# Kernel tuning notes

Measured on AMD Instinct MI355X. Metric: run time of the kernel, lower is better.

The kernel has to match this reference:

```python
import jax, jax.numpy as jnp
import numpy as np
import math

B, T, C = 2, 2048, 768
NH, HD = 12, 64  # n_head, head_dim

def setup_inputs() -> dict:
    key = jax.random.key(0)
    k1, k2, k3 = jax.random.split(key, 3)
    x = jax.random.normal(k1, (B, T, C), dtype=jnp.float32)
    mask = jnp.tril(jnp.ones((T, T), dtype=bool))[None, None]  # [1,1,T,T] causal
    Wqkv = jax.random.normal(k2, (C, 3 * C), dtype=jnp.float32) * (1.0 / math.sqrt(C))
    Wproj = jax.random.normal(k3, (C, C), dtype=jnp.float32) * (1.0 / math.sqrt(C))
    return {"x": x, "mask": mask, "Wqkv": Wqkv, "Wproj": Wproj}

def reference(x, mask, Wqkv, Wproj):
    b, t, c = x.shape
    qkv = x @ Wqkv  # [b,t,3c]
    q, k, v = jnp.split(qkv, 3, axis=-1)
    q = q.reshape(b, t, NH, HD).transpose(0, 2, 1, 3)  # [b,h,t,d]
    k = k.reshape(b, t, NH, HD).transpose(0, 2, 1, 3)
    v = v.reshape(b, t, NH, HD).transpose(0, 2, 1, 3)
    att = jnp.einsum('bhqd,bhkd->bhqk', q, k) / math.sqrt(HD)
    att = jnp.where(mask, att, -jnp.inf)
    att = jax.nn.softmax(att, axis=-1)
    out = jnp.einsum('bhqk,bhkd->bhqd', att, v)
    out = out.transpose(0, 2, 1, 3).reshape(b, t, c)
    return out @ Wproj
```

## Files before the change

### kernel.cpp

```cpp
#include <hip/hip_runtime.h>
#include <hip/hip_bf16.h>

#define T_   2048
#define C_   768
#define NH_  12
#define HD_  64
#define M_   (2*T_)
#define N1_  (3*C_)
#define PB_  ((size_t)NH_*T_*HD_)
#define KS_  0.180336880f

typedef __attribute__((ext_vector_type(8))) short  short8;
typedef __attribute__((ext_vector_type(4))) float  floatx4;

__device__ __forceinline__ floatx4 mfma_bf16(short8 a, short8 b, floatx4 c) {
    return __builtin_amdgcn_mfma_f32_16x16x32_bf16(a, b, c, 0, 0, 0);
}
__device__ __forceinline__ float fast_exp2(float x) {
    return __builtin_amdgcn_exp2f(x);
}

__global__ __launch_bounds__(256) void gemm_xw(const void* __restrict__ A,
                                               const float* __restrict__ Bf,
                                               int a_is_f32, int row0, int N, int K,
                                               int mode, int orow0,
                                               void* __restrict__ O0,
                                               __hip_bfloat16* __restrict__ O1,
                                               __hip_bfloat16* __restrict__ O2) {
    __shared__ __align__(16) __hip_bfloat16 As[128 * 40];
    __shared__ __align__(16) __hip_bfloat16 Bs[128 * 40];

    const int tid  = threadIdx.x;
    const int n0   = blockIdx.x * 128;
    const int m0   = blockIdx.y * 128;
    const int srow = tid >> 1;
    const int scol = (tid & 1) * 16;
    const int bn   = tid & 127;
    const int bg   = tid >> 7;
    const int wave = tid >> 6;
    const int ln   = tid & 63;
    const int l16  = ln & 15;
    const int q4   = ln >> 4;
    const int wm   = (wave >> 1) * 64;
    const int wn   = (wave & 1) * 64;

    floatx4 acc[4][4];
#pragma unroll
    for (int i = 0; i < 4; i++)
#pragma unroll
        for (int j = 0; j < 4; j++) acc[i][j] = (floatx4){0.f, 0.f, 0.f, 0.f};

    const size_t arow = (size_t)(row0 + m0 + srow) * K;

    for (int k0 = 0; k0 < K; k0 += 32) {
        union { __hip_bfloat16 h[16]; short8 v[2]; } au, bu;
        if (a_is_f32) {
            const float* Af = (const float*)A;
            const size_t base = arow + k0 + scol;
            floatx4 f0 = *(const floatx4*)(Af + base);
            floatx4 f1 = *(const floatx4*)(Af + base + 4);
            floatx4 f2 = *(const floatx4*)(Af + base + 8);
            floatx4 f3 = *(const floatx4*)(Af + base + 12);
#pragma unroll
            for (int j = 0; j < 4; j++) {
                au.h[j]      = __float2bfloat16(f0[j]);
                au.h[4 + j]  = __float2bfloat16(f1[j]);
                au.h[8 + j]  = __float2bfloat16(f2[j]);
                au.h[12 + j] = __float2bfloat16(f3[j]);
            }
        } else {
            const __hip_bfloat16* Ab = (const __hip_bfloat16*)A;
            au.v[0] = *(const short8*)(Ab + arow + k0 + scol);
            au.v[1] = *(const short8*)(Ab + arow + k0 + scol + 8);
        }
#pragma unroll
        for (int j = 0; j < 16; j++)
            bu.h[j] = __float2bfloat16(Bf[(size_t)(k0 + bg * 16 + j) * N + n0 + bn]);
        __syncthreads();
        *(short8*)(As + srow * 40 + scol)     = au.v[0];
        *(short8*)(As + srow * 40 + scol + 8) = au.v[1];
        *(short8*)(Bs + bn * 40 + bg * 16)     = bu.v[0];
        *(short8*)(Bs + bn * 40 + bg * 16 + 8) = bu.v[1];
        __syncthreads();
        short8 af[4], bfr[4];
#pragma unroll
        for (int i = 0; i < 4; i++) {
            af[i]  = *(const short8*)(As + (wm + i * 16 + l16) * 40 + q4 * 8);
            bfr[i] = *(const short8*)(Bs + (wn + i * 16 + l16) * 40 + q4 * 8);
        }
#pragma unroll
        for (int i = 0; i < 4; i++)
#pragma unroll
            for (int j = 0; j < 4; j++)
                acc[i][j] = mfma_bf16(af[i], bfr[j], acc[i][j]);
    }

#pragma unroll
    for (int i = 0; i < 4; i++) {
        const int mbase = m0 + wm + i * 16 + q4 * 4;
#pragma unroll
        for (int j = 0; j < 4; j++) {
            const int n = n0 + wn + j * 16 + l16;
#pragma unroll
            for (int r = 0; r < 4; r++) {
                const int mm = mbase + r;
                const float fv = acc[i][j][r];
                if (mode == 1) {
                    ((float*)O0)[(size_t)(orow0 + mm) * N + n] = fv;
                } else {
                    const __hip_bfloat16 hv = __float2bfloat16(fv);
                    const int which = n / C_;
                    const int rem   = n - which * C_;
                    const int h     = rem >> 6;
                    const int d     = rem & 63;
                    const int bh    = (mm >> 11) * NH_ + h;
                    const int t     = mm & (T_ - 1);
                    if (which == 0)      ((__hip_bfloat16*)O0)[((size_t)bh * T_ + t) * HD_ + d] = hv;
                    else if (which == 1) O1[((size_t)bh * T_ + t) * HD_ + d] = hv;
                    else                 O2[((size_t)bh * HD_ + d) * T_ + t] = hv;
                }
            }
        }
    }
}

__global__ __launch_bounds__(128) void attn_fused(const __hip_bfloat16* __restrict__ Q,
                                                  const __hip_bfloat16* __restrict__ Kd,
                                                  const __hip_bfloat16* __restrict__ Vt,
                                                  __hip_bfloat16* __restrict__ O) {
    __shared__ __align__(16) __hip_bfloat16 plds[2][2][16][72];
    __shared__ __align__(16) floatx4 accbuf[2][4][64];
    __shared__ float mbuf[2][16], lbuf[2][16];

    const int bh   = blockIdx.x;
    const int wid  = threadIdx.x >> 6;
    const int lane = threadIdx.x & 63;
    const int l16  = lane & 15;
    const int q4   = lane >> 4;
    const int i    = 63 - (int)blockIdx.y;
    const int q0A  = 32 * i;
    const int q0B  = 32 * i + 16;
    const int nch  = (i >> 1) + 1;

    const __hip_bfloat16* Qh = Q  + (size_t)bh * T_ * HD_;
    const __hip_bfloat16* Kh = Kd + (size_t)bh * T_ * HD_;
    const __hip_bfloat16* Vh = Vt + (size_t)bh * HD_ * T_;

    short8 aqA[2], aqB[2];
#pragma unroll
    for (int kt = 0; kt < 2; kt++) {
        aqA[kt] = *(const short8*)(Qh + (size_t)(q0A + l16) * HD_ + kt * 32 + q4 * 8);
        aqB[kt] = *(const short8*)(Qh + (size_t)(q0B + l16) * HD_ + kt * 32 + q4 * 8);
    }

    floatx4 accA[4], accB[4];
#pragma unroll
    for (int ct = 0; ct < 4; ct++) {
        accA[ct] = (floatx4){0.f, 0.f, 0.f, 0.f};
        accB[ct] = (floatx4){0.f, 0.f, 0.f, 0.f};
    }
    float mA[4], lA[4], mB[4], lB[4];
#pragma unroll
    for (int r = 0; r < 4; r++) { mA[r] = mB[r] = -3e38f; lA[r] = lB[r] = 0.f; }

    for (int c = wid; c < nch; c += 2) {
        const int kv0 = c * 64;
        const bool diag = (c == nch - 1);

        short8 bk[4][2];
#pragma unroll
        for (int nt = 0; nt < 4; nt++)
#pragma unroll
            for (int kt = 0; kt < 2; kt++)
                bk[nt][kt] = *(const short8*)(Kh + (size_t)(kv0 + nt * 16 + l16) * HD_ + kt * 32 + q4 * 8);

        floatx4 sA[4], sB[4];
#pragma unroll
        for (int nt = 0; nt < 4; nt++) {
            sA[nt] = (floatx4){0.f, 0.f, 0.f, 0.f};
            sB[nt] = (floatx4){0.f, 0.f, 0.f, 0.f};
#pragma unroll
            for (int kt = 0; kt < 2; kt++) {
                sA[nt] = mfma_bf16(aqA[kt], bk[nt][kt], sA[nt]);
                sB[nt] = mfma_bf16(aqB[kt], bk[nt][kt], sB[nt]);
            }
        }

        if (diag) {
#pragma unroll
            for (int r = 0; r < 4; r++) {
#pragma unroll
                for (int nt = 0; nt < 4; nt++) {
                    const int kvc = kv0 + nt * 16 + l16;
                    if (kvc > q0A + q4 * 4 + r) sA[nt][r] = -3e38f;
                    if (kvc > q0B + q4 * 4 + r) sB[nt][r] = -3e38f;
                }
            }
        }

        float mxA[4], mxB[4];
#pragma unroll
        for (int r = 0; r < 4; r++) {
            mxA[r] = fmaxf(fmaxf(sA[0][r], sA[1][r]), fmaxf(sA[2][r], sA[3][r]));
            mxB[r] = fmaxf(fmaxf(sB[0][r], sB[1][r]), fmaxf(sB[2][r], sB[3][r]));
        }
#pragma unroll
        for (int off = 1; off < 16; off <<= 1)
#pragma unroll
            for (int r = 0; r < 4; r++) {
                mxA[r] = fmaxf(mxA[r], __shfl_xor(mxA[r], off, 64));
                mxB[r] = fmaxf(mxB[r], __shfl_xor(mxB[r], off, 64));
            }

        float rsA[4], rsB[4], alA[4], alB[4];
#pragma unroll
        for (int r = 0; r < 4; r++) {
            const float mnA = fmaxf(mA[r], mxA[r]);
            const float mnB = fmaxf(mB[r], mxB[r]);
            alA[r] = fast_exp2((mA[r] - mnA) * KS_);
            alB[r] = fast_exp2((mB[r] - mnB) * KS_);
            mA[r] = mnA; mB[r] = mnB;
            const float mkA = mnA * KS_, mkB = mnB * KS_;
            float ra = 0.f, rb = 0.f;
#pragma unroll
            for (int nt = 0; nt < 4; nt++) {
                const float pa = fast_exp2(sA[nt][r] * KS_ - mkA);
                const float pb = fast_exp2(sB[nt][r] * KS_ - mkB);
                plds[wid][0][q4 * 4 + r][nt * 16 + l16] = __float2bfloat16(pa);
                plds[wid][1][q4 * 4 + r][nt * 16 + l16] = __float2bfloat16(pb);
                ra += pa; rb += pb;
            }
            rsA[r] = ra; rsB[r] = rb;
        }
#pragma unroll
        for (int off = 1; off < 16; off <<= 1)
#pragma unroll
            for (int r = 0; r < 4; r++) {
                rsA[r] += __shfl_xor(rsA[r], off, 64);
                rsB[r] += __shfl_xor(rsB[r], off, 64);
            }
#pragma unroll
        for (int r = 0; r < 4; r++) {
            lA[r] = alA[r] * lA[r] + rsA[r];
            lB[r] = alB[r] * lB[r] + rsB[r];
        }
#pragma unroll
        for (int ct = 0; ct < 4; ct++)
#pragma unroll
            for (int r = 0; r < 4; r++) {
                accA[ct][r] *= alA[r];
                accB[ct][r] *= alB[r];
            }

        __threadfence_block();

        short8 apA[2], apB[2];
#pragma unroll
        for (int kt = 0; kt < 2; kt++) {
            apA[kt] = *(const short8*)(&plds[wid][0][l16][kt * 32 + q4 * 8]);
            apB[kt] = *(const short8*)(&plds[wid][1][l16][kt * 32 + q4 * 8]);
        }
#pragma unroll
        for (int ct = 0; ct < 4; ct++)
#pragma unroll
            for (int kt = 0; kt < 2; kt++) {
                short8 bv = *(const short8*)(Vh + (size_t)(ct * 16 + l16) * T_ + kv0 + kt * 32 + q4 * 8);
                accA[ct] = mfma_bf16(apA[kt], bv, accA[ct]);
                accB[ct] = mfma_bf16(apB[kt], bv, accB[ct]);
            }

        __threadfence_block();
    }

    __syncthreads();
    if (wid == 0) {
        if (l16 == 0)
#pragma unroll
            for (int r = 0; r < 4; r++) { mbuf[1][q4 * 4 + r] = mB[r]; lbuf[1][q4 * 4 + r] = lB[r]; }
#pragma unroll
        for (int ct = 0; ct < 4; ct++) accbuf[1][ct][lane] = accB[ct];
    } else {
        if (l16 == 0)
#pragma unroll
            for (int r = 0; r < 4; r++) { mbuf[0][q4 * 4 + r] = mA[r]; lbuf[0][q4 * 4 + r] = lA[r]; }
#pragma unroll
        for (int ct = 0; ct < 4; ct++) accbuf[0][ct][lane] = accA[ct];
    }
    __syncthreads();

    const int orow0 = (bh / NH_) * T_;
    const int hcol  = (bh % NH_) * HD_;
    const int slot  = wid;
    const int q0    = wid ? q0B : q0A;
#pragma unroll
    for (int r = 0; r < 4; r++) {
        const float m0v = wid ? mB[r] : mA[r];
        const float l0v = wid ? lB[r] : lA[r];
        const float m1v = mbuf[slot][q4 * 4 + r];
        const float l1v = lbuf[slot][q4 * 4 + r];
        const float ms  = fmaxf(m0v, m1v);
        const float w0  = fast_exp2((m0v - ms) * KS_);
        const float w1  = fast_exp2((m1v - ms) * KS_);
        const float inv = 1.0f / (l0v * w0 + l1v * w1);
        __hip_bfloat16* orow = O + (size_t)(orow0 + q0 + q4 * 4 + r) * C_ + hcol;
#pragma unroll
        for (int ct = 0; ct < 4; ct++) {
            const float a0 = wid ? accB[ct][r] : accA[ct][r];
            const float a1 = accbuf[slot][ct][lane][r];
            orow[ct * 16 + l16] = __float2bfloat16((a0 * w0 + a1 * w1) * inv);
        }
    }
}

extern "C" void kernel_launch(void* const* d_in, const int* in_sizes, int n_in,
                              void* d_out, int out_size, void* d_ws, size_t ws_size,
                              hipStream_t stream) {
    const float *x = nullptr, *wqkv = nullptr, *wproj = nullptr;
    for (int i = 0; i < n_in; i++) {
        const int s = in_sizes[i];
        if (s == M_ * C_ && !x) x = (const float*)d_in[i];
        else if (s == C_ * N1_ && !wqkv) wqkv = (const float*)d_in[i];
        else if (s == C_ * C_ && !wproj) wproj = (const float*)d_in[i];
    }
    float* out = (float*)d_out;
    __hip_bfloat16* ws = (__hip_bfloat16*)d_ws;
    __hip_bfloat16* Vt = (__hip_bfloat16*)d_out;

    const size_t needB = 6 * PB_ * 2;
    if (ws_size >= needB) {
        __hip_bfloat16* Qall = ws;
        __hip_bfloat16* Kall = Qall + 2 * PB_;
        __hip_bfloat16* ATT  = Kall + 2 * PB_;
        gemm_xw<<<dim3(N1_ / 128, M_ / 128), 256, 0, stream>>>(
            x, wqkv, 1, 0, N1_, C_, 0, 0, (void*)Qall, Kall, Vt);
        attn_fused<<<dim3(2 * NH_, 64), 128, 0, stream>>>(Qall, Kall, Vt, ATT);
        gemm_xw<<<dim3(C_ / 128, M_ / 128), 256, 0, stream>>>(
            ATT, wproj, 0, 0, C_, C_, 1, 0, (void*)out, nullptr, nullptr);
    } else {
        __hip_bfloat16* Qb      = ws;
        __hip_bfloat16* Kb      = Qb + PB_;
        __hip_bfloat16* ATTb[2] = {Kb + PB_, Kb + 2 * PB_};
        for (int b = 0; b < 2; b++) {
            __hip_bfloat16* Vtb = Vt + (size_t)b * PB_;
            gemm_xw<<<dim3(N1_ / 128, T_ / 128), 256, 0, stream>>>(
                x, wqkv, 1, b * T_, N1_, C_, 0, 0, (void*)Qb, Kb, Vtb);
            attn_fused<<<dim3(NH_, 64), 128, 0, stream>>>(Qb, Kb, Vtb, ATTb[b]);
        }
        for (int b = 0; b < 2; b++)
            gemm_xw<<<dim3(C_ / 128, T_ / 128), 256, 0, stream>>>(
                ATTb[b], wproj, 0, 0, C_, C_, 1, b * T_, (void*)out, nullptr, nullptr);
    }
}
```

Before: 212.9 us.

## Pre-convert inputs to bf16, add transposed-B GEMMs, split attention across four waves

Adds prep kernels that convert x to bf16 and transpose-convert both weight matrices to bf16, so the GEMMs load contiguous bf16 rows and skip the per-tile strided fp32 weight reads and conversions. The QKV GEMM becomes a 128x128 transposed-B kernel and the output projection a 64x64 tile kernel for more blocks. Attention goes from two to four waves per block with a tree merge of partial softmax states through reused LDS. The cost is extra launches and extra global traffic for the converted copies, which are stored in reused workspace and output buffers.

```diff
diff --git a/kernel.cpp b/kernel.cpp
--- a/kernel.cpp
+++ b/kernel.cpp
@@ -11,6 +11,7 @@
 #define KS_  0.180336880f
 
 typedef __attribute__((ext_vector_type(8))) short  short8;
+typedef __attribute__((ext_vector_type(4))) short  shortx4;
 typedef __attribute__((ext_vector_type(4))) float  floatx4;
 
 __device__ __forceinline__ floatx4 mfma_bf16(short8 a, short8 b, floatx4 c) {
@@ -18,6 +19,185 @@
 }
 __device__ __forceinline__ float fast_exp2(float x) {
     return __builtin_amdgcn_exp2f(x);
+}
+
+__global__ __launch_bounds__(256) void prep1(const float* __restrict__ x,
+                                             const float* __restrict__ wqkv,
+                                             __hip_bfloat16* __restrict__ xb,
+                                             __hip_bfloat16* __restrict__ wqkvT) {
+    if (blockIdx.x < 3072) {
+        const int idx = blockIdx.x * 256 + threadIdx.x;
+        const floatx4 v = ((const floatx4*)x)[idx];
+        union { __hip_bfloat16 h[4]; shortx4 s; } u;
+#pragma unroll
+        for (int j = 0; j < 4; j++) u.h[j] = __float2bfloat16(v[j]);
+        ((shortx4*)xb)[idx] = u.s;
+    } else {
+        const int j  = (blockIdx.x - 3072) * 256 + threadIdx.x;
+        const int k8 = j / N1_;
+        const int n  = j - k8 * N1_;
+        union { __hip_bfloat16 h[8]; short8 s; } u;
+#pragma unroll
+        for (int jj = 0; jj < 8; jj++)
+            u.h[jj] = __float2bfloat16(wqkv[(size_t)(k8 * 8 + jj) * N1_ + n]);
+        *(short8*)(wqkvT + (size_t)n * C_ + k8 * 8) = u.s;
+    }
+}
+
+__global__ __launch_bounds__(256) void prep2(const float* __restrict__ wproj,
+                                             __hip_bfloat16* __restrict__ wprojT) {
+    const int j  = blockIdx.x * 256 + threadIdx.x;
+    const int k8 = j / C_;
+    const int n  = j - k8 * C_;
+    union { __hip_bfloat16 h[8]; short8 s; } u;
+#pragma unroll
+    for (int jj = 0; jj < 8; jj++)
+        u.h[jj] = __float2bfloat16(wproj[(size_t)(k8 * 8 + jj) * C_ + n]);
+    *(short8*)(wprojT + (size_t)n * C_ + k8 * 8) = u.s;
+}
+
+__global__ __launch_bounds__(256) void gemm_bt128(const __hip_bfloat16* __restrict__ A,
+                                                  const __hip_bfloat16* __restrict__ Bt,
+                                                  int N, int K, int mode,
+                                                  void* __restrict__ O0,
+                                                  __hip_bfloat16* __restrict__ O1,
+                                                  __hip_bfloat16* __restrict__ O2) {
+    __shared__ __align__(16) __hip_bfloat16 As[128 * 40];
+    __shared__ __align__(16) __hip_bfloat16 Bs[128 * 40];
+
+    const int tid  = threadIdx.x;
+    const int n0   = blockIdx.x * 128;
+    const int m0   = blockIdx.y * 128;
+    const int srow = tid >> 1;
+    const int scol = (tid & 1) * 16;
+    const int wave = tid >> 6;
+    const int ln   = tid & 63;
+    const int l16  = ln & 15;
+    const int q4   = ln >> 4;
+    const int wm   = (wave >> 1) * 64;
+    const int wn   = (wave & 1) * 64;
+
+    floatx4 acc[4][4];
+#pragma unroll
+    for (int i = 0; i < 4; i++)
+#pragma unroll
+        for (int j = 0; j < 4; j++) acc[i][j] = (floatx4){0.f, 0.f, 0.f, 0.f};
+
+    const __hip_bfloat16* Ap = A  + (size_t)(m0 + srow) * K + scol;
+    const __hip_bfloat16* Bp = Bt + (size_t)(n0 + srow) * K + scol;
+
+    for (int k0 = 0; k0 < K; k0 += 32) {
+        short8 a0 = *(const short8*)(Ap + k0);
+        short8 a1 = *(const short8*)(Ap + k0 + 8);
+        short8 b0 = *(const short8*)(Bp + k0);
+        short8 b1 = *(const short8*)(Bp + k0 + 8);
+        __syncthreads();
+        *(short8*)(As + srow * 40 + scol)     = a0;
+        *(short8*)(As + srow * 40 + scol + 8) = a1;
+        *(short8*)(Bs + srow * 40 + scol)     = b0;
+        *(short8*)(Bs + srow * 40 + scol + 8) = b1;
+        __syncthreads();
+        short8 af[4], bfr[4];
+#pragma unroll
+        for (int i = 0; i < 4; i++) {
+            af[i]  = *(const short8*)(As + (wm + i * 16 + l16) * 40 + q4 * 8);
+            bfr[i] = *(const short8*)(Bs + (wn + i * 16 + l16) * 40 + q4 * 8);
+        }
+#pragma unroll
+        for (int i = 0; i < 4; i++)
+#pragma unroll
+            for (int j = 0; j < 4; j++)
+                acc[i][j] = mfma_bf16(af[i], bfr[j], acc[i][j]);
+    }
+
+#pragma unroll
+    for (int i = 0; i < 4; i++) {
+        const int mbase = m0 + wm + i * 16 + q4 * 4;
+#pragma unroll
+        for (int j = 0; j < 4; j++) {
+            const int n = n0 + wn + j * 16 + l16;
+#pragma unroll
+            for (int r = 0; r < 4; r++) {
+                const int mm = mbase + r;
+                const float fv = acc[i][j][r];
+                if (mode == 1) {
+                    ((float*)O0)[(size_t)mm * N + n] = fv;
+                } else {
+                    const __hip_bfloat16 hv = __float2bfloat16(fv);
+                    const int which = n / C_;
+                    const int rem   = n - which * C_;
+                    const int h     = rem >> 6;
+                    const int d     = rem & 63;
+                    const int bh    = (mm >> 11) * NH_ + h;
+                    const int t     = mm & (T_ - 1);
+                    if (which == 0)      ((__hip_bfloat16*)O0)[((size_t)bh * T_ + t) * HD_ + d] = hv;
+                    else if (which == 1) O1[((size_t)bh * T_ + t) * HD_ + d] = hv;
+                    else                 O2[((size_t)bh * HD_ + d) * T_ + t] = hv;
+                }
+            }
+        }
+    }
+}
+
+__global__ __launch_bounds__(256) void gemm_bt64(const __hip_bfloat16* __restrict__ A,
+                                                 const __hip_bfloat16* __restrict__ Bt,
+                                                 int N, int K,
+                                                 float* __restrict__ O0) {
+    __shared__ __align__(16) __hip_bfloat16 As[64 * 40];
+    __shared__ __align__(16) __hip_bfloat16 Bs[64 * 40];
+
+    const int tid  = threadIdx.x;
+    const int n0   = blockIdx.x * 64;
+    const int m0   = blockIdx.y * 64;
+    const int srow = tid >> 2;
+    const int scol = (tid & 3) * 8;
+    const int wave = tid >> 6;
+    const int ln   = tid & 63;
+    const int l16  = ln & 15;
+    const int q4   = ln >> 4;
+    const int wm   = (wave >> 1) * 32;
+    const int wn   = (wave & 1) * 32;
+
+    floatx4 acc[2][2];
+#pragma unroll
+    for (int i = 0; i < 2; i++)
+#pragma unroll
+        for (int j = 0; j < 2; j++) acc[i][j] = (floatx4){0.f, 0.f, 0.f, 0.f};
+
+    const __hip_bfloat16* Ap = A  + (size_t)(m0 + srow) * K + scol;
+    const __hip_bfloat16* Bp = Bt + (size_t)(n0 + srow) * K + scol;
+
+    for (int k0 = 0; k0 < K; k0 += 32) {
+        short8 av = *(const short8*)(Ap + k0);
+        short8 bv = *(const short8*)(Bp + k0);
+        __syncthreads();
+        *(short8*)(As + srow * 40 + scol) = av;
+        *(short8*)(Bs + srow * 40 + scol) = bv;
+        __syncthreads();
+        short8 af[2], bfr[2];
+#pragma unroll
+        for (int i = 0; i < 2; i++) {
+            af[i]  = *(const short8*)(As + (wm + i * 16 + l16) * 40 + q4 * 8);
+            bfr[i] = *(const short8*)(Bs + (wn + i * 16 + l16) * 40 + q4 * 8);
+        }
+#pragma unroll
+        for (int i = 0; i < 2; i++)
+#pragma unroll
+            for (int j = 0; j < 2; j++)
+                acc[i][j] = mfma_bf16(af[i], bfr[j], acc[i][j]);
+    }
+
+#pragma unroll
+    for (int i = 0; i < 2; i++) {
+        const int mbase = m0 + wm + i * 16 + q4 * 4;
+#pragma unroll
+        for (int j = 0; j < 2; j++) {
+            const int n = n0 + wn + j * 16 + l16;
+#pragma unroll
+            for (int r = 0; r < 4; r++)
+                O0[(size_t)(mbase + r) * N + n] = acc[i][j][r];
+        }
+    }
 }
 
 __global__ __launch_bounds__(256) void gemm_xw(const void* __restrict__ A,
@@ -77,8 +257,8 @@
         for (int j = 0; j < 16; j++)
             bu.h[j] = __float2bfloat16(Bf[(size_t)(k0 + bg * 16 + j) * N + n0 + bn]);
         __syncthreads();
-        *(short8*)(As + srow * 40 + scol)     = au.v[0];
-        *(short8*)(As + srow * 40 + scol + 8) = au.v[1];
+        *(short8*)(As + srow * 40 + scol)      = au.v[0];
+        *(short8*)(As + srow * 40 + scol + 8)  = au.v[1];
         *(short8*)(Bs + bn * 40 + bg * 16)     = bu.v[0];
         *(short8*)(Bs + bn * 40 + bg * 16 + 8) = bu.v[1];
         __syncthreads();
@@ -124,13 +304,11 @@
     }
 }
 
-__global__ __launch_bounds__(128) void attn_fused(const __hip_bfloat16* __restrict__ Q,
+__global__ __launch_bounds__(256) void attn_fused(const __hip_bfloat16* __restrict__ Q,
                                                   const __hip_bfloat16* __restrict__ Kd,
                                                   const __hip_bfloat16* __restrict__ Vt,
                                                   __hip_bfloat16* __restrict__ O) {
-    __shared__ __align__(16) __hip_bfloat16 plds[2][2][16][72];
-    __shared__ __align__(16) floatx4 accbuf[2][4][64];
-    __shared__ float mbuf[2][16], lbuf[2][16];
+    __shared__ __align__(16) __hip_bfloat16 plds[4][2][16][72];
 
     const int bh   = blockIdx.x;
     const int wid  = threadIdx.x >> 6;
@@ -163,7 +341,7 @@
 #pragma unroll
     for (int r = 0; r < 4; r++) { mA[r] = mB[r] = -3e38f; lA[r] = lB[r] = 0.f; }
 
-    for (int c = wid; c < nch; c += 2) {
+    for (int c = wid; c < nch; c += 4) {
         const int kv0 = c * 64;
         const bool diag = (c == nch - 1);
 
@@ -273,41 +451,68 @@
     }
 
     __syncthreads();
+    floatx4* accbuf = (floatx4*)&plds[0][0][0][0];
+    float*   mlbuf  = (float*)((char*)&plds[0][0][0][0] + 16384);
+
+    auto publish = [&](int slot) {
+#pragma unroll
+        for (int ct = 0; ct < 4; ct++) {
+            accbuf[((slot * 2 + 0) * 4 + ct) * 64 + lane] = accA[ct];
+            accbuf[((slot * 2 + 1) * 4 + ct) * 64 + lane] = accB[ct];
+        }
+        if (l16 == 0) {
+#pragma unroll
+            for (int r = 0; r < 4; r++) {
+                mlbuf[((slot * 2 + 0) * 2 + 0) * 16 + q4 * 4 + r] = mA[r];
+                mlbuf[((slot * 2 + 0) * 2 + 1) * 16 + q4 * 4 + r] = lA[r];
+                mlbuf[((slot * 2 + 1) * 2 + 0) * 16 + q4 * 4 + r] = mB[r];
+                mlbuf[((slot * 2 + 1) * 2 + 1) * 16 + q4 * 4 + r] = lB[r];
+            }
+        }
+    };
+    auto mergeIn = [&](int slot) {
+#pragma unroll
+        for (int r = 0; r < 4; r++) {
+            const float m1A = mlbuf[((slot * 2 + 0) * 2 + 0) * 16 + q4 * 4 + r];
+            const float l1A = mlbuf[((slot * 2 + 0) * 2 + 1) * 16 + q4 * 4 + r];
+            const float m1B = mlbuf[((slot * 2 + 1) * 2 + 0) * 16 + q4 * 4 + r];
+            const float l1B = mlbuf[((slot * 2 + 1) * 2 + 1) * 16 + q4 * 4 + r];
+            const float MA = fmaxf(mA[r], m1A), MB = fmaxf(mB[r], m1B);
+            const float w0A = fast_exp2((mA[r] - MA) * KS_);
+            const float w1A = fast_exp2((m1A  - MA) * KS_);
+            const float w0B = fast_exp2((mB[r] - MB) * KS_);
+            const float w1B = fast_exp2((m1B  - MB) * KS_);
+            mA[r] = MA; lA[r] = w0A * lA[r] + w1A * l1A;
+            mB[r] = MB; lB[r] = w0B * lB[r] + w1B * l1B;
+#pragma unroll
+            for (int ct = 0; ct < 4; ct++) {
+                accA[ct][r] = w0A * accA[ct][r] + w1A * accbuf[((slot * 2 + 0) * 4 + ct) * 64 + lane][r];
+                accB[ct][r] = w0B * accB[ct][r] + w1B * accbuf[((slot * 2 + 1) * 4 + ct) * 64 + lane][r];
+            }
+        }
+    };
+
+    if (wid >= 2) publish(wid - 2);
+    __syncthreads();
+    if (wid < 2) mergeIn(wid);
+    __syncthreads();
+    if (wid == 1) publish(0);
+    __syncthreads();
     if (wid == 0) {
-        if (l16 == 0)
-#pragma unroll
-            for (int r = 0; r < 4; r++) { mbuf[1][q4 * 4 + r] = mB[r]; lbuf[1][q4 * 4 + r] = lB[r]; }
-#pragma unroll
-        for (int ct = 0; ct < 4; ct++) accbuf[1][ct][lane] = accB[ct];
-    } else {
-        if (l16 == 0)
-#pragma unroll
-            for (int r = 0; r < 4; r++) { mbuf[0][q4 * 4 + r] = mA[r]; lbuf[0][q4 * 4 + r] = lA[r]; }
-#pragma unroll
-        for (int ct = 0; ct < 4; ct++) accbuf[0][ct][lane] = accA[ct];
-    }
-    __syncthreads();
-
-    const int orow0 = (bh / NH_) * T_;
-    const int hcol  = (bh % NH_) * HD_;
-    const int slot  = wid;
-    const int q0    = wid ? q0B : q0A;
-#pragma unroll
-    for (int r = 0; r < 4; r++) {
-        const float m0v = wid ? mB[r] : mA[r];
-        const float l0v = wid ? lB[r] : lA[r];
-        const float m1v = mbuf[slot][q4 * 4 + r];
-        const float l1v = lbuf[slot][q4 * 4 + r];
-        const float ms  = fmaxf(m0v, m1v);
-        const float w0  = fast_exp2((m0v - ms) * KS_);
-        const float w1  = fast_exp2((m1v - ms) * KS_);
-        const float inv = 1.0f / (l0v * w0 + l1v * w1);
-        __hip_bfloat16* orow = O + (size_t)(orow0 + q0 + q4 * 4 + r) * C_ + hcol;
-#pragma unroll
-        for (int ct = 0; ct < 4; ct++) {
-            const float a0 = wid ? accB[ct][r] : accA[ct][r];
-            const float a1 = accbuf[slot][ct][lane][r];
-            orow[ct * 16 + l16] = __float2bfloat16((a0 * w0 + a1 * w1) * inv);
+        mergeIn(0);
+        const int orow0 = (bh / NH_) * T_;
+        const int hcol  = (bh % NH_) * HD_;
+#pragma unroll
+        for (int r = 0; r < 4; r++) {
+            const float invA = 1.0f / lA[r];
+            const float invB = 1.0f / lB[r];
+            __hip_bfloat16* oA = O + (size_t)(orow0 + q0A + q4 * 4 + r) * C_ + hcol;
+            __hip_bfloat16* oB = O + (size_t)(orow0 + q0B + q4 * 4 + r) * C_ + hcol;
+#pragma unroll
+            for (int ct = 0; ct < 4; ct++) {
+                oA[ct * 16 + l16] = __float2bfloat16(accA[ct][r] * invA);
+                oB[ct * 16 + l16] = __float2bfloat16(accB[ct][r] * invB);
+            }
         }
     }
 }
@@ -328,14 +533,18 @@
 
     const size_t needB = 6 * PB_ * 2;
     if (ws_size >= needB) {
-        __hip_bfloat16* Qall = ws;
-        __hip_bfloat16* Kall = Qall + 2 * PB_;
-        __hip_bfloat16* ATT  = Kall + 2 * PB_;
-        gemm_xw<<<dim3(N1_ / 128, M_ / 128), 256, 0, stream>>>(
-            x, wqkv, 1, 0, N1_, C_, 0, 0, (void*)Qall, Kall, Vt);
-        attn_fused<<<dim3(2 * NH_, 64), 128, 0, stream>>>(Qall, Kall, Vt, ATT);
-        gemm_xw<<<dim3(C_ / 128, M_ / 128), 256, 0, stream>>>(
-            ATT, wproj, 0, 0, C_, C_, 1, 0, (void*)out, nullptr, nullptr);
+        __hip_bfloat16* Qall   = ws;
+        __hip_bfloat16* Kall   = Qall + 2 * PB_;
+        __hip_bfloat16* ATT    = Kall + 2 * PB_;
+        __hip_bfloat16* xb     = ATT;
+        __hip_bfloat16* wqkvT  = (__hip_bfloat16*)d_out + 2 * PB_;
+        __hip_bfloat16* wprojT = Qall;
+        prep1<<<dim3(3936), 256, 0, stream>>>(x, wqkv, xb, wqkvT);
+        gemm_bt128<<<dim3(N1_ / 128, M_ / 128), 256, 0, stream>>>(
+            xb, wqkvT, N1_, C_, 0, (void*)Qall, Kall, Vt);
+        attn_fused<<<dim3(2 * NH_, 64), 256, 0, stream>>>(Qall, Kall, Vt, ATT);
+        prep2<<<dim3(288), 256, 0, stream>>>(wproj, wprojT);
+        gemm_bt64<<<dim3(C_ / 64, M_ / 64), 256, 0, stream>>>(ATT, wprojT, C_, C_, out);
     } else {
         __hip_bfloat16* Qb      = ws;
         __hip_bfloat16* Kb      = Qb + PB_;
@@ -344,7 +553,7 @@
             __hip_bfloat16* Vtb = Vt + (size_t)b * PB_;
             gemm_xw<<<dim3(N1_ / 128, T_ / 128), 256, 0, stream>>>(
                 x, wqkv, 1, b * T_, N1_, C_, 0, 0, (void*)Qb, Kb, Vtb);
-            attn_fused<<<dim3(NH_, 64), 128, 0, stream>>>(Qb, Kb, Vtb, ATTb[b]);
+            attn_fused<<<dim3(NH_, 64), 256, 0, stream>>>(Qb, Kb, Vtb, ATTb[b]);
         }
         for (int b = 0; b < 2; b++)
             gemm_xw<<<dim3(C_ / 128, T_ / 128), 256, 0, stream>>>(
```

After: 212.8 us. Within noise of the previous version (-0.1%).
